# Optimization experiments

Measured on AMD Instinct MI355X. Metric: run time of the kernel, lower is better.

Reference implementation:

```python
import jax, jax.numpy as jnp
import numpy as np

H = 8      # head_nums
D = 64     # head_planes
SCALE = D ** -0.5


def setup_inputs() -> dict:
    key = jax.random.key(0)
    ks = jax.random.split(key, 7)
    B, Nq, Nkv = 2, 2048, 2048
    Cq, Ck, I = 1024, 768, H * D
    return {
        "x": jax.random.normal(ks[0], (B, Nq, Cq), jnp.float32),
        "context": jax.random.normal(ks[1], (B, Nkv, Ck), jnp.float32),
        "Wq": jax.random.normal(ks[2], (Cq, I), jnp.float32) * (Cq ** -0.5),
        "Wk": jax.random.normal(ks[3], (Ck, I), jnp.float32) * (Ck ** -0.5),
        "Wv": jax.random.normal(ks[4], (Ck, I), jnp.float32) * (Ck ** -0.5),
        "Wo": jax.random.normal(ks[5], (I, Cq), jnp.float32) * (I ** -0.5),
        "bo": jnp.zeros((Cq,), jnp.float32),
    }


def reference(x, context, Wq, Wk, Wv, Wo, bo):
    B, Nq, _ = x.shape
    Nkv = context.shape[1]
    # projections (bias-free, as in to_q/to_k/to_v)
    q = (x @ Wq).reshape(B, Nq, H, D)        # b i h d
    k = (context @ Wk).reshape(B, Nkv, H, D)  # b j h d
    v = (context @ Wv).reshape(B, Nkv, H, D)
    # scaled dot-product attention, full [B,H,Nq,Nkv] scores as in original
    sim = jnp.einsum('bihd,bjhd->bhij', q, k) * SCALE
    attn = jax.nn.softmax(sim, axis=-1)
    out = jnp.einsum('bhij,bjhd->bihd', attn, v).reshape(B, Nq, H * D)
    # to_out linear (dropout_prob=0.0 -> identity)
    return out @ Wo + bo
```

## Files before the change

kernel.cpp:

```cpp
#include <hip/hip_runtime.h>
#include <hip/hip_bf16.h>

typedef __hip_bfloat16 bf16;
typedef __attribute__((ext_vector_type(8))) short short8;
typedef __attribute__((ext_vector_type(4))) float f32x4;

#define MFMA16(a, b, c) __builtin_amdgcn_mfma_f32_16x16x32_bf16((a), (b), (c), 0, 0, 0)

#define BATCH 2
#define NQ 2048
#define NKV 2048
#define HEADS 8
#define DHEAD 64
#define CQ 1024
#define CK 768
#define IDIM 512
#define SCALE 0.125f

__device__ __forceinline__ short8 ld8(const bf16* p) {
    return *(const short8*)p;
}

__device__ __forceinline__ void async_ld16(const bf16* g, bf16* l) {
    __builtin_amdgcn_global_load_lds((__attribute__((address_space(1))) const void*)g,
                                     (__attribute__((address_space(3))) void*)l,
                                     16, 0, 0);
}

__global__ __launch_bounds__(256) void prologue(
    const float* __restrict__ x, const float* __restrict__ ctx,
    const float* __restrict__ Wq, const float* __restrict__ Wk,
    const float* __restrict__ Wv, const float* __restrict__ Wo,
    bf16* __restrict__ Xb, bf16* __restrict__ Cb,
    bf16* __restrict__ WqT, bf16* __restrict__ WkT,
    bf16* __restrict__ WvT, bf16* __restrict__ WoT) {
    __shared__ float tile[64][65];
    const int t = threadIdx.x;
    const int bx = blockIdx.x;

    if (bx < 3584) {
        int idx = bx * 256 + t;
        const int NX8 = (4096 * 1024) / 8;
        const float4* srcp;
        bf16* dstp;
        if (idx < NX8) {
            srcp = (const float4*)x + (size_t)idx * 2;
            dstp = Xb + (size_t)idx * 8;
        } else {
            int j = idx - NX8;
            srcp = (const float4*)ctx + (size_t)j * 2;
            dstp = Cb + (size_t)j * 8;
        }
        float4 v0 = srcp[0], v1 = srcp[1];
        bf16 tmp[8] = {__float2bfloat16(v0.x), __float2bfloat16(v0.y),
                       __float2bfloat16(v0.z), __float2bfloat16(v0.w),
                       __float2bfloat16(v1.x), __float2bfloat16(v1.y),
                       __float2bfloat16(v1.z), __float2bfloat16(v1.w)};
        *(short8*)dstp = *(short8*)tmp;
        return;
    }

    int tb = bx - 3584;
    const float* src; bf16* dst; int R, C, ti;
    if (tb < 128)      { src = Wq; dst = WqT; R = 1024; C = 512;  ti = tb; }
    else if (tb < 224) { src = Wk; dst = WkT; R = 768;  C = 512;  ti = tb - 128; }
    else if (tb < 320) { src = Wv; dst = WvT; R = 768;  C = 512;  ti = tb - 224; }
    else               { src = Wo; dst = WoT; R = 512;  C = 1024; ti = tb - 320; }
    const int tilesC = C >> 6;
    const int tr = ti / tilesC, tc = ti - tr * tilesC;

    {
        int row = t >> 4;
        int c4 = (t & 15) * 4;
#pragma unroll
        for (int p = 0; p < 4; ++p) {
            float4 v = *(const float4*)&src[(size_t)(tr * 64 + p * 16 + row) * C + tc * 64 + c4];
            tile[p * 16 + row][c4 + 0] = v.x;
            tile[p * 16 + row][c4 + 1] = v.y;
            tile[p * 16 + row][c4 + 2] = v.z;
            tile[p * 16 + row][c4 + 3] = v.w;
        }
    }
    __syncthreads();
    {
        int oc = t >> 2;
        int r0 = (t & 3) * 16;
        bf16 tmp[16];
#pragma unroll
        for (int j = 0; j < 16; ++j)
            tmp[j] = __float2bfloat16(tile[r0 + j][oc]);
        bf16* dp = dst + (size_t)(tc * 64 + oc) * R + tr * 64 + r0;
        *(short8*)dp = *(short8*)&tmp[0];
        *(short8*)(dp + 8) = *(short8*)&tmp[8];
    }
}

__global__ __launch_bounds__(256) void qkv_gemm(
    const bf16* __restrict__ Xb, const bf16* __restrict__ Cb,
    const bf16* __restrict__ WqT, const bf16* __restrict__ WkT,
    const bf16* __restrict__ WvT,
    bf16* __restrict__ Qb, bf16* __restrict__ Kb, bf16* __restrict__ Vt) {
    __shared__ bf16 At[2][64 * 64];
    __shared__ bf16 Bts[2][128 * 64];

    const int z = blockIdx.z;
    const bf16* A  = (z == 0) ? Xb : Cb;
    const bf16* Bt = (z == 0) ? WqT : (z == 1) ? WkT : WvT;
    const int K = (z == 0) ? 1024 : 768;

    const int t = threadIdx.x;
    const int wave = t >> 6;
    const int lane = t & 63;
    const int n15 = lane & 15;
    const int quad = lane >> 4;
    const int wm = wave >> 1;
    const int wn = wave & 1;
    const int bm = blockIdx.y;
    const int bn = blockIdx.x;

    f32x4 acc[2][4] = {};

    const bf16* Ablk = A + (size_t)bm * 64 * K;
    const bf16* Bblk = Bt + (size_t)bn * 128 * K;

    int ar[2], ac[2], br[4], bc[4];
#pragma unroll
    for (int i = 0; i < 2; ++i) {
        int g = i * 256 + t;
        ar[i] = g >> 3; ac[i] = ((g & 7) ^ (ar[i] & 7)) * 8;
    }
#pragma unroll
    for (int i = 0; i < 4; ++i) {
        int g = i * 256 + t;
        br[i] = g >> 3; bc[i] = ((g & 7) ^ (br[i] & 7)) * 8;
    }

#pragma unroll
    for (int i = 0; i < 2; ++i)
        async_ld16(Ablk + ar[i] * K + ac[i], &At[0][(i * 256 + t) * 8]);
#pragma unroll
    for (int i = 0; i < 4; ++i)
        async_ld16(Bblk + br[i] * K + bc[i], &Bts[0][(i * 256 + t) * 8]);
    __syncthreads();

    for (int k0 = 0; k0 < K; k0 += 64) {
        const int p = (k0 >> 6) & 1;
        if (k0 + 64 < K) {
            const int q = p ^ 1;
            const int kn = k0 + 64;
#pragma unroll
            for (int i = 0; i < 2; ++i)
                async_ld16(Ablk + ar[i] * K + kn + ac[i], &At[q][(i * 256 + t) * 8]);
#pragma unroll
            for (int i = 0; i < 4; ++i)
                async_ld16(Bblk + br[i] * K + kn + bc[i], &Bts[q][(i * 256 + t) * 8]);
        }

#pragma unroll
        for (int kh = 0; kh < 2; ++kh) {
            short8 af[2], bfr[4];
#pragma unroll
            for (int mt = 0; mt < 2; ++mt) {
                int R = wm * 32 + mt * 16 + n15;
                af[mt] = ld8(&At[p][R * 64 + (((kh * 4 + quad) ^ (R & 7)) * 8)]);
            }
#pragma unroll
            for (int nt = 0; nt < 4; ++nt) {
                int R = wn * 64 + nt * 16 + n15;
                bfr[nt] = ld8(&Bts[p][R * 64 + (((kh * 4 + quad) ^ (R & 7)) * 8)]);
            }
#pragma unroll
            for (int mt = 0; mt < 2; ++mt)
#pragma unroll
                for (int nt = 0; nt < 4; ++nt)
                    acc[mt][nt] = MFMA16(af[mt], bfr[nt], acc[mt][nt]);
        }

        __syncthreads();
    }

    bf16* C = (z == 0) ? Qb : (z == 1) ? Kb : Vt;
#pragma unroll
    for (int mt = 0; mt < 2; ++mt) {
#pragma unroll
        for (int nt = 0; nt < 4; ++nt) {
            int col = bn * 128 + wn * 64 + nt * 16 + n15;
#pragma unroll
            for (int r = 0; r < 4; ++r) {
                int row = bm * 64 + wm * 32 + mt * 16 + quad * 4 + r;
                bf16 v = __float2bfloat16(acc[mt][nt][r]);
                if (z < 2) {
                    C[(size_t)row * 512 + col] = v;
                } else {
                    int b = row >> 11, j = row & 2047;
                    int h = col >> 6, d = col & 63;
                    C[(size_t)(((b << 3) + h) * 64 + d) * 2048 + j] = v;
                }
            }
        }
    }
}

__global__ __launch_bounds__(256) void out_gemm(const bf16* __restrict__ A,
                                                const bf16* __restrict__ Bt,
                                                const float* __restrict__ bias,
                                                float* __restrict__ C) {
    const int K = 512, N = 1024;
    __shared__ bf16 At[2][64 * 64];
    __shared__ bf16 Bts[2][128 * 64];

    const int t = threadIdx.x;
    const int wave = t >> 6;
    const int lane = t & 63;
    const int n15 = lane & 15;
    const int quad = lane >> 4;
    const int wm = wave >> 1;
    const int wn = wave & 1;
    const int bm = blockIdx.y;
    const int bn = blockIdx.x;

    f32x4 acc[2][4] = {};

    const bf16* Ablk = A + (size_t)bm * 64 * K;
    const bf16* Bblk = Bt + (size_t)bn * 128 * K;

    int ar[2], ac[2], br[4], bc[4];
#pragma unroll
    for (int i = 0; i < 2; ++i) {
        int g = i * 256 + t;
        ar[i] = g >> 3; ac[i] = ((g & 7) ^ (ar[i] & 7)) * 8;
    }
#pragma unroll
    for (int i = 0; i < 4; ++i) {
        int g = i * 256 + t;
        br[i] = g >> 3; bc[i] = ((g & 7) ^ (br[i] & 7)) * 8;
    }

#pragma unroll
    for (int i = 0; i < 2; ++i)
        async_ld16(Ablk + ar[i] * K + ac[i], &At[0][(i * 256 + t) * 8]);
#pragma unroll
    for (int i = 0; i < 4; ++i)
        async_ld16(Bblk + br[i] * K + bc[i], &Bts[0][(i * 256 + t) * 8]);
    __syncthreads();

    for (int k0 = 0; k0 < K; k0 += 64) {
        const int p = (k0 >> 6) & 1;
        if (k0 + 64 < K) {
            const int q = p ^ 1;
            const int kn = k0 + 64;
#pragma unroll
            for (int i = 0; i < 2; ++i)
                async_ld16(Ablk + ar[i] * K + kn + ac[i], &At[q][(i * 256 + t) * 8]);
#pragma unroll
            for (int i = 0; i < 4; ++i)
                async_ld16(Bblk + br[i] * K + kn + bc[i], &Bts[q][(i * 256 + t) * 8]);
        }

#pragma unroll
        for (int kh = 0; kh < 2; ++kh) {
            short8 af[2], bfr[4];
#pragma unroll
            for (int mt = 0; mt < 2; ++mt) {
                int R = wm * 32 + mt * 16 + n15;
                af[mt] = ld8(&At[p][R * 64 + (((kh * 4 + quad) ^ (R & 7)) * 8)]);
            }
#pragma unroll
            for (int nt = 0; nt < 4; ++nt) {
                int R = wn * 64 + nt * 16 + n15;
                bfr[nt] = ld8(&Bts[p][R * 64 + (((kh * 4 + quad) ^ (R & 7)) * 8)]);
            }
#pragma unroll
            for (int mt = 0; mt < 2; ++mt)
#pragma unroll
                for (int nt = 0; nt < 4; ++nt)
                    acc[mt][nt] = MFMA16(af[mt], bfr[nt], acc[mt][nt]);
        }

        __syncthreads();
    }

#pragma unroll
    for (int mt = 0; mt < 2; ++mt) {
#pragma unroll
        for (int nt = 0; nt < 4; ++nt) {
            int col = bn * 128 + wn * 64 + nt * 16 + n15;
            float bv = bias[col];
#pragma unroll
            for (int r = 0; r < 4; ++r) {
                int row = bm * 64 + wm * 32 + mt * 16 + quad * 4 + r;
                C[(size_t)row * N + col] = acc[mt][nt][r] + bv;
            }
        }
    }
}

__global__ __launch_bounds__(512, 1) void flash_attn(const bf16* __restrict__ Q,
                                                     const bf16* __restrict__ K,
                                                     const bf16* __restrict__ Vt,
                                                     bf16* __restrict__ O) {
    __shared__ bf16 Kt[2][64 * 64];
    __shared__ bf16 Vte[2][64 * 64];
    __shared__ bf16 Pa[8][16 * 72];
    __shared__ float Oc[4][64][16];
    __shared__ float Lc[4][16];

    const int t = threadIdx.x;
    const int wave = t >> 6;
    const int g = wave >> 1;
    const int khalf = wave & 1;
    const int lane = t & 63;
    const int n15 = lane & 15;
    const int quad = lane >> 4;

    const int L = blockIdx.x;
    const int bh = L & 15;
    const int b = bh >> 3, h = bh & 7;
    const int q0 = (L >> 4) * 64;
    const int qw = q0 + g * 16;

    const bf16* Qp = Q + ((size_t)(b * NQ + qw) * IDIM + h * DHEAD);
    const bf16* Kp = K + ((size_t)b * NKV * IDIM + h * DHEAD)
                       + (size_t)(khalf * 1024) * IDIM;
    const bf16* Vp = Vt + (size_t)((b * HEADS + h) * DHEAD) * NKV + khalf * 1024;
    bf16* Pw = Pa[wave];

    short8 qa0 = ld8(Qp + n15 * IDIM + quad * 8);
    short8 qa1 = ld8(Qp + n15 * IDIM + 32 + quad * 8);

    const int s0 = g * 128 + lane;
    const int s1 = s0 + 64;
    const int r0 = s0 >> 3, c0 = (s0 & 7) ^ (r0 & 7);
    const int r1 = s1 >> 3, c1 = (s1 & 7) ^ (r1 & 7);
    const bf16* kg0 = Kp + r0 * IDIM + c0 * 8;
    const bf16* kg1 = Kp + r1 * IDIM + c1 * 8;
    const bf16* vg0 = Vp + (size_t)r0 * NKV + c0 * 8;
    const bf16* vg1 = Vp + (size_t)r1 * NKV + c1 * 8;
    bf16* kl0 = &Kt[khalf][s0 * 8];
    bf16* kl1 = &Kt[khalf][s1 * 8];
    bf16* vl0 = &Vte[khalf][s0 * 8];
    bf16* vl1 = &Vte[khalf][s1 * 8];

    f32x4 o[4] = {};
    float lsum = 0.f;
    const int sw = n15 & 7;

    for (int key0 = 0; key0 < 1024; key0 += 64) {
        async_ld16(kg0 + (size_t)key0 * IDIM, kl0);
        async_ld16(kg1 + (size_t)key0 * IDIM, kl1);
        async_ld16(vg0 + key0, vl0);
        async_ld16(vg1 + key0, vl1);
        __syncthreads();

        f32x4 s[4] = {};
#pragma unroll
        for (int su = 0; su < 4; ++su) {
            const bf16* kr = &Kt[khalf][(su * 16 + n15) * 64];
            short8 ka0 = ld8(kr + ((quad ^ sw) * 8));
            short8 ka1 = ld8(kr + (((4 + quad) ^ sw) * 8));
            s[su] = MFMA16(ka0, qa0, s[su]);
            s[su] = MFMA16(ka1, qa1, s[su]);
        }

#pragma unroll
        for (int su = 0; su < 4; ++su) {
            float p0 = __expf(s[su][0] * SCALE);
            float p1 = __expf(s[su][1] * SCALE);
            float p2 = __expf(s[su][2] * SCALE);
            float p3 = __expf(s[su][3] * SCALE);
            lsum += (p0 + p1) + (p2 + p3);
            bf16 pk[4] = {__float2bfloat16(p0), __float2bfloat16(p1),
                          __float2bfloat16(p2), __float2bfloat16(p3)};
            *(uint2*)&Pw[n15 * 72 + su * 16 + quad * 4] = *(uint2*)pk;
        }
        asm volatile("s_waitcnt lgkmcnt(0)" ::: "memory");

        short8 pb0 = ld8(&Pw[n15 * 72 + quad * 8]);
        short8 pb1 = ld8(&Pw[n15 * 72 + 32 + quad * 8]);

#pragma unroll
        for (int d4 = 0; d4 < 4; ++d4) {
            const bf16* vr = &Vte[khalf][(d4 * 16 + n15) * 64];
            short8 va0 = ld8(vr + ((quad ^ sw) * 8));
            short8 va1 = ld8(vr + (((4 + quad) ^ sw) * 8));
            o[d4] = MFMA16(va0, pb0, o[d4]);
            o[d4] = MFMA16(va1, pb1, o[d4]);
        }
        __syncthreads();
    }

    lsum += __shfl_xor(lsum, 16, 64);
    lsum += __shfl_xor(lsum, 32, 64);

    if (khalf == 1) {
#pragma unroll
        for (int d4 = 0; d4 < 4; ++d4)
#pragma unroll
            for (int r = 0; r < 4; ++r)
                Oc[g][d4 * 16 + quad * 4 + r][n15] = o[d4][r];
        if (quad == 0) Lc[g][n15] = lsum;
    }
    __syncthreads();
    if (khalf == 0) {
        float lt = lsum + Lc[g][n15];
        float inv = 1.0f / lt;
#pragma unroll
        for (int d4 = 0; d4 < 4; ++d4) {
            bf16 pk[4];
#pragma unroll
            for (int r = 0; r < 4; ++r) {
                float v = o[d4][r] + Oc[g][d4 * 16 + quad * 4 + r][n15];
                pk[r] = __float2bfloat16(v * inv);
            }
            *(uint2*)&Pa[g][n15 * 72 + d4 * 16 + quad * 4] = *(uint2*)pk;
        }
    }
    __syncthreads();

    {
        int ql = t >> 3, seg = t & 7;
        const bf16* src = &Pa[ql >> 4][(ql & 15) * 72 + seg * 8];
        short8 a0 = ld8(src);
        bf16* dst = O + ((size_t)(b * NQ + q0 + ql) * IDIM + h * DHEAD + seg * 8);
        *(short8*)dst = a0;
    }
}

extern "C" void kernel_launch(void* const* d_in, const int* in_sizes, int n_in,
                              void* d_out, int out_size, void* d_ws, size_t ws_size,
                              hipStream_t stream) {
    (void)in_sizes; (void)n_in; (void)out_size; (void)ws_size;

    const float* x   = (const float*)d_in[0];
    const float* ctx = (const float*)d_in[1];
    const float* Wq  = (const float*)d_in[2];
    const float* Wk  = (const float*)d_in[3];
    const float* Wv  = (const float*)d_in[4];
    const float* Wo  = (const float*)d_in[5];
    const float* bo  = (const float*)d_in[6];
    float* out = (float*)d_out;

    char* ws = (char*)d_ws;
    bf16* Xb  = (bf16*)(ws + 0);
    bf16* Cb  = (bf16*)(ws + 8388608);
    bf16* WqT = (bf16*)(ws + 14680064);
    bf16* WkT = (bf16*)(ws + 15728640);
    bf16* WvT = (bf16*)(ws + 16515072);
    bf16* WoT = (bf16*)(ws + 17301504);
    bf16* Qb  = (bf16*)(ws + 18350080);
    bf16* Kb  = (bf16*)(ws + 22544384);
    bf16* Vt  = (bf16*)(ws + 26738688);
    bf16* Ob  = (bf16*)(ws + 30932992);

    prologue<<<4032, 256, 0, stream>>>(x, ctx, Wq, Wk, Wv, Wo,
                                       Xb, Cb, WqT, WkT, WvT, WoT);

    qkv_gemm<<<dim3(4, 64, 3), 256, 0, stream>>>(Xb, Cb, WqT, WkT, WvT, Qb, Kb, Vt);

    flash_attn<<<512, 512, 0, stream>>>(Qb, Kb, Vt, Ob);

    out_gemm<<<dim3(8, 64), 256, 0, stream>>>(Ob, WoT, bo, out);
}
```

Measured before the change: 149.2 us.

## Use 32x32 MFMA with 128-query tiles and double-buffered K/V in attention

The flash attention kernel now gives each wave 32 query rows and uses 32x32x16 bf16 MFMAs in place of 16x16x32, doubling the query tile per block to 128 and halving the grid to 256 blocks. K/V tiles are double-buffered in LDS so the next tile's async load is issued before computing the current one. The aim is more reuse of each loaded K/V tile and overlap of global loads with compute. The cost is fewer blocks on the GPU, which may underfill the compute units, plus more LDS and registers per block.

Measured after the change: 152.5 us. +2.2%, slower.

```diff
diff --git a/kernel.cpp b/kernel.cpp
--- a/kernel.cpp
+++ b/kernel.cpp
@@ -4,8 +4,10 @@
 typedef __hip_bfloat16 bf16;
 typedef __attribute__((ext_vector_type(8))) short short8;
 typedef __attribute__((ext_vector_type(4))) float f32x4;
+typedef __attribute__((ext_vector_type(16))) float f32x16;
 
 #define MFMA16(a, b, c) __builtin_amdgcn_mfma_f32_16x16x32_bf16((a), (b), (c), 0, 0, 0)
+#define MFMA32(a, b, c) __builtin_amdgcn_mfma_f32_32x32x16_bf16((a), (b), (c), 0, 0, 0)
 
 #define BATCH 2
 #define NQ 2048
@@ -299,130 +301,154 @@
                                                      const bf16* __restrict__ K,
                                                      const bf16* __restrict__ Vt,
                                                      bf16* __restrict__ O) {
-    __shared__ bf16 Kt[2][64 * 64];
-    __shared__ bf16 Vte[2][64 * 64];
-    __shared__ bf16 Pa[8][16 * 72];
-    __shared__ float Oc[4][64][16];
-    __shared__ float Lc[4][16];
+    __shared__ bf16 Kt[2][2][64 * 64];
+    __shared__ bf16 Vte[2][2][64 * 64];
+    __shared__ bf16 Pa[8][32 * 72];
+    __shared__ float Lc[4][32];
 
     const int t = threadIdx.x;
     const int wave = t >> 6;
     const int g = wave >> 1;
-    const int khalf = wave & 1;
+    const int kh = wave & 1;
     const int lane = t & 63;
-    const int n15 = lane & 15;
-    const int quad = lane >> 4;
+    const int n31 = lane & 31;
+    const int half = lane >> 5;
 
     const int L = blockIdx.x;
     const int bh = L & 15;
     const int b = bh >> 3, h = bh & 7;
-    const int q0 = (L >> 4) * 64;
-    const int qw = q0 + g * 16;
+    const int q0 = (L >> 4) * 128;
+    const int qw = q0 + g * 32;
 
     const bf16* Qp = Q + ((size_t)(b * NQ + qw) * IDIM + h * DHEAD);
     const bf16* Kp = K + ((size_t)b * NKV * IDIM + h * DHEAD)
-                       + (size_t)(khalf * 1024) * IDIM;
-    const bf16* Vp = Vt + (size_t)((b * HEADS + h) * DHEAD) * NKV + khalf * 1024;
+                       + (size_t)(kh * 1024) * IDIM;
+    const bf16* Vp = Vt + (size_t)((b * HEADS + h) * DHEAD) * NKV + kh * 1024;
     bf16* Pw = Pa[wave];
 
-    short8 qa0 = ld8(Qp + n15 * IDIM + quad * 8);
-    short8 qa1 = ld8(Qp + n15 * IDIM + 32 + quad * 8);
-
-    const int s0 = g * 128 + lane;
-    const int s1 = s0 + 64;
+    short8 qa[4];
+#pragma unroll
+    for (int ks = 0; ks < 4; ++ks)
+        qa[ks] = ld8(Qp + n31 * IDIM + ks * 16 + half * 8);
+
+    const int u = g * 64 + lane;
+    const int s0 = u, s1 = u + 256;
     const int r0 = s0 >> 3, c0 = (s0 & 7) ^ (r0 & 7);
     const int r1 = s1 >> 3, c1 = (s1 & 7) ^ (r1 & 7);
     const bf16* kg0 = Kp + r0 * IDIM + c0 * 8;
     const bf16* kg1 = Kp + r1 * IDIM + c1 * 8;
     const bf16* vg0 = Vp + (size_t)r0 * NKV + c0 * 8;
     const bf16* vg1 = Vp + (size_t)r1 * NKV + c1 * 8;
-    bf16* kl0 = &Kt[khalf][s0 * 8];
-    bf16* kl1 = &Kt[khalf][s1 * 8];
-    bf16* vl0 = &Vte[khalf][s0 * 8];
-    bf16* vl1 = &Vte[khalf][s1 * 8];
-
-    f32x4 o[4] = {};
+
+    f32x16 o[2] = {};
     float lsum = 0.f;
-    const int sw = n15 & 7;
+
+    async_ld16(kg0, &Kt[0][kh][s0 * 8]);
+    async_ld16(kg1, &Kt[0][kh][s1 * 8]);
+    async_ld16(vg0, &Vte[0][kh][s0 * 8]);
+    async_ld16(vg1, &Vte[0][kh][s1 * 8]);
+    __syncthreads();
 
     for (int key0 = 0; key0 < 1024; key0 += 64) {
-        async_ld16(kg0 + (size_t)key0 * IDIM, kl0);
-        async_ld16(kg1 + (size_t)key0 * IDIM, kl1);
-        async_ld16(vg0 + key0, vl0);
-        async_ld16(vg1 + key0, vl1);
+        const int p = (key0 >> 6) & 1;
+        if (key0 + 64 < 1024) {
+            const int q = p ^ 1;
+            const int kn = key0 + 64;
+            async_ld16(kg0 + (size_t)kn * IDIM, &Kt[q][kh][s0 * 8]);
+            async_ld16(kg1 + (size_t)kn * IDIM, &Kt[q][kh][s1 * 8]);
+            async_ld16(vg0 + kn, &Vte[q][kh][s0 * 8]);
+            async_ld16(vg1 + kn, &Vte[q][kh][s1 * 8]);
+        }
+
+        f32x16 s[2] = {};
+#pragma unroll
+        for (int su = 0; su < 2; ++su) {
+            const int row = su * 32 + n31;
+            const bf16* kr = &Kt[p][kh][row * 64];
+            const int rs = row & 7;
+#pragma unroll
+            for (int ks = 0; ks < 4; ++ks) {
+                short8 ka = ld8(kr + (((ks * 2 + half) ^ rs) * 8));
+                s[su] = MFMA32(ka, qa[ks], s[su]);
+            }
+        }
+
+#pragma unroll
+        for (int su = 0; su < 2; ++su) {
+#pragma unroll
+            for (int rg = 0; rg < 4; ++rg) {
+                float p0 = __expf(s[su][rg * 4 + 0] * SCALE);
+                float p1 = __expf(s[su][rg * 4 + 1] * SCALE);
+                float p2 = __expf(s[su][rg * 4 + 2] * SCALE);
+                float p3 = __expf(s[su][rg * 4 + 3] * SCALE);
+                lsum += (p0 + p1) + (p2 + p3);
+                bf16 pk[4] = {__float2bfloat16(p0), __float2bfloat16(p1),
+                              __float2bfloat16(p2), __float2bfloat16(p3)};
+                *(uint2*)&Pw[n31 * 72 + su * 32 + rg * 8 + half * 4] = *(uint2*)pk;
+            }
+        }
+        asm volatile("s_waitcnt lgkmcnt(0)" ::: "memory");
+
+        short8 pb[4];
+#pragma unroll
+        for (int ks2 = 0; ks2 < 4; ++ks2)
+            pb[ks2] = ld8(&Pw[n31 * 72 + ks2 * 16 + half * 8]);
+
+#pragma unroll
+        for (int dt = 0; dt < 2; ++dt) {
+            const int row = dt * 32 + n31;
+            const bf16* vr = &Vte[p][kh][row * 64];
+            const int rs = row & 7;
+#pragma unroll
+            for (int ks2 = 0; ks2 < 4; ++ks2) {
+                short8 va = ld8(vr + (((ks2 * 2 + half) ^ rs) * 8));
+                o[dt] = MFMA32(va, pb[ks2], o[dt]);
+            }
+        }
         __syncthreads();
-
-        f32x4 s[4] = {};
-#pragma unroll
-        for (int su = 0; su < 4; ++su) {
-            const bf16* kr = &Kt[khalf][(su * 16 + n15) * 64];
-            short8 ka0 = ld8(kr + ((quad ^ sw) * 8));
-            short8 ka1 = ld8(kr + (((4 + quad) ^ sw) * 8));
-            s[su] = MFMA16(ka0, qa0, s[su]);
-            s[su] = MFMA16(ka1, qa1, s[su]);
-        }
-
-#pragma unroll
-        for (int su = 0; su < 4; ++su) {
-            float p0 = __expf(s[su][0] * SCALE);
-            float p1 = __expf(s[su][1] * SCALE);
-            float p2 = __expf(s[su][2] * SCALE);
-            float p3 = __expf(s[su][3] * SCALE);
-            lsum += (p0 + p1) + (p2 + p3);
-            bf16 pk[4] = {__float2bfloat16(p0), __float2bfloat16(p1),
-                          __float2bfloat16(p2), __float2bfloat16(p3)};
-            *(uint2*)&Pw[n15 * 72 + su * 16 + quad * 4] = *(uint2*)pk;
-        }
-        asm volatile("s_waitcnt lgkmcnt(0)" ::: "memory");
-
-        short8 pb0 = ld8(&Pw[n15 * 72 + quad * 8]);
-        short8 pb1 = ld8(&Pw[n15 * 72 + 32 + quad * 8]);
-
-#pragma unroll
-        for (int d4 = 0; d4 < 4; ++d4) {
-            const bf16* vr = &Vte[khalf][(d4 * 16 + n15) * 64];
-            short8 va0 = ld8(vr + ((quad ^ sw) * 8));
-            short8 va1 = ld8(vr + (((4 + quad) ^ sw) * 8));
-            o[d4] = MFMA16(va0, pb0, o[d4]);
-            o[d4] = MFMA16(va1, pb1, o[d4]);
-        }
-        __syncthreads();
-    }
-
-    lsum += __shfl_xor(lsum, 16, 64);
+    }
+
     lsum += __shfl_xor(lsum, 32, 64);
 
-    if (khalf == 1) {
-#pragma unroll
-        for (int d4 = 0; d4 < 4; ++d4)
-#pragma unroll
-            for (int r = 0; r < 4; ++r)
-                Oc[g][d4 * 16 + quad * 4 + r][n15] = o[d4][r];
-        if (quad == 0) Lc[g][n15] = lsum;
-    }
-    __syncthreads();
-    if (khalf == 0) {
-        float lt = lsum + Lc[g][n15];
-        float inv = 1.0f / lt;
-#pragma unroll
-        for (int d4 = 0; d4 < 4; ++d4) {
-            bf16 pk[4];
-#pragma unroll
-            for (int r = 0; r < 4; ++r) {
-                float v = o[d4][r] + Oc[g][d4 * 16 + quad * 4 + r][n15];
-                pk[r] = __float2bfloat16(v * inv);
-            }
-            *(uint2*)&Pa[g][n15 * 72 + d4 * 16 + quad * 4] = *(uint2*)pk;
+    float* Comb = (float*)&Kt[0][0][0];
+    if (kh == 1) {
+#pragma unroll
+        for (int dt = 0; dt < 2; ++dt)
+#pragma unroll
+            for (int r = 0; r < 16; ++r) {
+                int d = dt * 32 + (r & 3) + 8 * (r >> 2) + 4 * half;
+                Comb[((g * 64 + d) << 5) + n31] = o[dt][r];
+            }
+        if (lane < 32) Lc[g][lane] = lsum;
+    }
+    __syncthreads();
+    if (kh == 0) {
+        float inv = 1.0f / (lsum + Lc[g][n31]);
+#pragma unroll
+        for (int dt = 0; dt < 2; ++dt) {
+#pragma unroll
+            for (int rg = 0; rg < 4; ++rg) {
+                int db = dt * 32 + rg * 8 + half * 4;
+                bf16 pk[4];
+#pragma unroll
+                for (int i = 0; i < 4; ++i) {
+                    float v = o[dt][rg * 4 + i] + Comb[((g * 64 + db + i) << 5) + n31];
+                    pk[i] = __float2bfloat16(v * inv);
+                }
+                *(uint2*)&Pa[g * 2][n31 * 72 + db] = *(uint2*)pk;
+            }
         }
     }
     __syncthreads();
 
     {
-        int ql = t >> 3, seg = t & 7;
-        const bf16* src = &Pa[ql >> 4][(ql & 15) * 72 + seg * 8];
+        int ql = t >> 2, seg = t & 3;
+        const bf16* src = &Pa[(ql >> 5) * 2][(ql & 31) * 72 + seg * 16];
         short8 a0 = ld8(src);
-        bf16* dst = O + ((size_t)(b * NQ + q0 + ql) * IDIM + h * DHEAD + seg * 8);
+        short8 a1 = ld8(src + 8);
+        bf16* dst = O + ((size_t)(b * NQ + q0 + ql) * IDIM + h * DHEAD + seg * 16);
         *(short8*)dst = a0;
+        *(short8*)(dst + 8) = a1;
     }
 }
 
@@ -457,7 +483,7 @@
 
     qkv_gemm<<<dim3(4, 64, 3), 256, 0, stream>>>(Xb, Cb, WqT, WkT, WvT, Qb, Kb, Vt);
 
-    flash_attn<<<512, 512, 0, stream>>>(Qb, Kb, Vt, Ob);
+    flash_attn<<<256, 512, 0, stream>>>(Qb, Kb, Vt, Ob);
 
     out_gemm<<<dim3(8, 64), 256, 0, stream>>>(Ob, WoT, bo, out);
 }
```
